# Performance work log

Hardware: AMD Instinct MI355X
Metric: run time of the kernel (lower is better)

Reference implementation:

```python
import jax, jax.numpy as jnp
import numpy as np

SIZES = (20, 20, 20, 20, 20)          # formula_oh_sizes
OH_N = sum(SIZES)                      # 100
NUM_BINS = 65536                       # spect_bin.get_num_bins()
EPS_SIZE = 1e-4                        # eps added to subset size
IN_EPS = 1e-5                          # torch InstanceNorm1d default eps


def thermometer_oh(counts):
    # StructuredOneHot with accum=True: per-element thermometer encoding.
    # counts: (N, E) element counts -> (N, sum(SIZES)) with out[j]=1 iff j < count.
    outs = [(jnp.arange(s, dtype=counts.dtype)[None, :] < counts[:, i:i + 1]).astype(jnp.float32)
            for i, s in enumerate(SIZES)]
    return jnp.concatenate(outs, axis=-1)


def inorm(x):
    # InstanceNorm1d (affine=False) as applied here: normalize over last dim per row.
    m = jnp.mean(x, axis=-1, keepdims=True)
    v = jnp.var(x, axis=-1, keepdims=True)
    return (x - m) * jax.lax.rsqrt(v + IN_EPS)


def _lin(key, fan_in, fan_out):
    k1, k2 = jax.random.split(key)
    bound = 1.0 / np.sqrt(fan_in)
    W = jax.random.uniform(k1, (fan_in, fan_out), jnp.float32, -bound, bound)
    b = jax.random.uniform(k2, (fan_out,), jnp.float32, -bound, bound)
    return W, b


def setup_inputs():
    key = jax.random.key(0)
    ks = jax.random.split(key, 12)
    B, A, GF, S, P, E, D = 8, 48, 256, 4096, 32, 5, 256
    vert_feat_in = jax.random.normal(ks[0], (B, A, GF), jnp.float32)
    vert_mask_in = jnp.ones((B, A), jnp.float32)
    elem_idx = jax.random.randint(ks[1], (B, A), 0, E)
    vert_element_oh = jax.nn.one_hot(elem_idx, E, dtype=jnp.float32)
    adj_oh = jnp.zeros((B, A, A), jnp.float32)                      # unused by forward path
    atom_subsets = jax.random.randint(ks[2], (B, S, A), 0, 2).astype(jnp.int32)
    atom_subsets_peaks = jnp.zeros((1,), jnp.float32)               # unused (mass_idx/intensity used)
    mass_idx = jax.random.randint(ks[3], (B, S, P), 0, NUM_BINS).astype(jnp.int32)
    intensity = jax.random.uniform(ks[4], (B, S, P), jnp.float32)
    combine_W, combine_b = _lin(ks[5], OH_N + GF, GF)
    l1_W, l1_b = _lin(ks[6], GF, D)
    l2a_W, l2a_b = _lin(ks[7], D, D)
    l2b_W, l2b_b = _lin(ks[8], D, D)
    score_W, score_b = _lin(ks[9], D, 1)
    return {
        'vert_feat_in': vert_feat_in, 'vert_mask_in': vert_mask_in,
        'vert_element_oh': vert_element_oh, 'adj_oh': adj_oh,
        'atom_subsets': atom_subsets, 'atom_subsets_peaks': atom_subsets_peaks,
        'mass_idx': mass_idx, 'intensity': intensity,
        'combine_W': combine_W, 'combine_b': combine_b,
        'l1_W': l1_W, 'l1_b': l1_b, 'l2a_W': l2a_W, 'l2a_b': l2a_b,
        'l2b_W': l2b_W, 'l2b_b': l2b_b, 'score_W': score_W, 'score_b': score_b,
    }


def reference(vert_feat_in, vert_mask_in, vert_element_oh, adj_oh, atom_subsets,
              atom_subsets_peaks, mass_idx, intensity,
              combine_W, combine_b, l1_W, l1_b, l2a_W, l2a_b, l2b_W, l2b_b,
              score_W, score_b):
    B, A, GF = vert_feat_in.shape
    _, S, _ = atom_subsets.shape
    subsets_f = atom_subsets.astype(jnp.float32)
    masked_vert = vert_feat_in * vert_mask_in[:, :, None]               # (B,A,GF)
    subsets_masked = subsets_f * vert_mask_in[:, None, :]               # (B,S,A)
    # weighted sum of vertex features over each subset
    sws = jnp.einsum('bag,bsa->bsg', masked_vert, subsets_masked)        # (B,S,GF)
    # per-subset element counts -> structured one-hot formula encoding
    counts = jnp.einsum('bae,bsa->bse', vert_element_oh, subsets_f)      # (B,S,E)
    pf_oh = thermometer_oh(counts.reshape(-1, counts.shape[-1])).reshape(B, S, OH_N)
    subset_size = jnp.sum(subsets_masked, axis=2) + EPS_SIZE             # (B,S)
    mean_feat = sws / subset_size[:, :, None]
    normed = inorm(mean_feat)                                            # subset_weighted_norm
    combined = jax.nn.relu(jnp.concatenate([pf_oh, normed], -1) @ combine_W + combine_b)
    x = inorm(combined)                                                  # norm_post_combine
    x = jax.nn.relu(x @ l1_W + l1_b)
    x = jax.nn.leaky_relu(x @ l2a_W + l2a_b)
    x = jax.nn.leaky_relu(x @ l2b_W + l2b_b)
    x = jax.nn.relu(x)
    x = inorm(x)                                                         # norm_pre_score
    scores = (x @ score_W + score_b)[..., 0]                             # (B,S)
    probs = jax.nn.softmax(scores, axis=-1)
    # per-batch sparse mass-matrix binning: scatter-add intensity*prob into spectral bins
    weighted = intensity * probs[:, :, None]                             # (B,S,P)
    seg = jax.vmap(lambda idx, w: jax.ops.segment_sum(w, idx, num_segments=NUM_BINS))
    spect_out = seg(mass_idx.reshape(B, -1), weighted.reshape(B, -1))    # (B,NUM_BINS)
    return spect_out, probs
```

## Files before the change

### kernel.cpp

```cpp
#include <hip/hip_runtime.h>
#include <math.h>

#define B_DIM 8
#define A_DIM 48
#define GF_DIM 256
#define S_DIM 4096
#define P_DIM 32
#define E_DIM 5
#define OHN 100
#define NBINS 65536

typedef __attribute__((ext_vector_type(8))) short short8v;
typedef __attribute__((ext_vector_type(4))) float float4v;

__device__ __forceinline__ float wave_sum(float v) {
#pragma unroll
    for (int o = 32; o; o >>= 1) v += __shfl_xor(v, o, 64);
    return v;
}
__device__ __forceinline__ float wave_max(float v) {
#pragma unroll
    for (int o = 32; o; o >>= 1) v = fmaxf(v, __shfl_xor(v, o, 64));
    return v;
}
__device__ __forceinline__ float quad16_sum(float v) {
    v += __shfl_xor(v, 1, 64); v += __shfl_xor(v, 2, 64);
    v += __shfl_xor(v, 4, 64); v += __shfl_xor(v, 8, 64);
    return v;
}
__device__ __forceinline__ unsigned short bf16_rn(float x) {
    unsigned int u = __float_as_uint(x);
    return (unsigned short)((u + 0x7FFFu + ((u >> 16) & 1u)) >> 16);
}
__device__ __forceinline__ float bf16_val(unsigned short h) {
    return __uint_as_float(((unsigned int)h) << 16);
}
__device__ __forceinline__ float4v mfma_bf16(short8v a, short8v b, float4v c) {
    return __builtin_amdgcn_mfma_f32_16x16x32_bf16(a, b, c, 0, 0, 0);
}

__global__ __launch_bounds__(256) void k_prep(
    const float* __restrict__ cW, const float* __restrict__ l1W,
    const float* __restrict__ l2aW, const float* __restrict__ l2bW,
    const float* __restrict__ vert_feat, const float* __restrict__ vert_mask,
    const float* __restrict__ elem_oh,
    short* __restrict__ wp, short* __restrict__ wv,
    float* __restrict__ maskB, int* __restrict__ eiB,
    float4* __restrict__ spect4)
{
    const int blk = blockIdx.x;
    const int tid = threadIdx.x;
    if (blk < 1152) {
        int e = blk * 256 + tid;
        int c = e >> 13;
        int i = e & 8191;
        int j    = i & 7;
        int lane = (i >> 3) & 63;
        int nt   = (i >> 9) & 1;
        int wn   = i >> 10;
        int krel = (lane >> 4) * 8 + j;
        int n    = wn * 32 + nt * 16 + (lane & 15);
        float val = 0.f;
        if (c < 12) {
            int kp = c * 32 + krel;
            if (kp < 100)       val = cW[kp * 256 + n];
            else if (kp >= 128) val = cW[(kp - 28) * 256 + n];
        } else {
            int L  = (c - 12) >> 3;
            int kc = (c - 12) & 7;
            const float* W = (L == 0) ? l1W : (L == 1) ? l2aW : l2bW;
            val = W[(kc * 32 + krel) * 256 + n];
        }
        unsigned short h = bf16_rn(val);
        float lo = val - bf16_val(h);
        int base = c * 16384 + (i & 511);
        wp[base + (wn * 4 + nt) * 512]     = (short)h;
        wp[base + (wn * 4 + 2 + nt) * 512] = (short)bf16_rn(lo);
    } else if (blk < 1664) {
        int vb = blk - 1152;
        int vc = vb >> 5;
        int i  = (vb & 31) * 256 + tid;
        int b  = vc >> 1, v = vc & 1;
        int j    = i & 7;
        int lane = (i >> 3) & 63;
        int nt   = (i >> 9) & 1;
        int wn   = i >> 10;
        int k = v * 32 + (lane >> 4) * 8 + j;
        int n = wn * 32 + nt * 16 + (lane & 15);
        float val = 0.f;
        if (k < A_DIM) {
            float mk = vert_mask[b * A_DIM + k];
            val = vert_feat[((size_t)(b * A_DIM + k)) * GF_DIM + n] * mk * mk;
        }
        unsigned short h = bf16_rn(val);
        float lo = val - bf16_val(h);
        int base = vc * 16384 + (i & 511);
        wv[base + (wn * 4 + nt) * 512]     = (short)h;
        wv[base + (wn * 4 + 2 + nt) * 512] = (short)bf16_rn(lo);
    } else if (blk == 1664) {
        for (int t = tid; t < B_DIM * A_DIM; t += 256) {
            maskB[t] = vert_mask[t];
            int ei = 0;
#pragma unroll
            for (int e = 0; e < E_DIM; ++e)
                if (elem_oh[t * E_DIM + e] > 0.5f) ei = e;
            eiB[t] = ei;
        }
    } else {
        int z = (blk - 1665) * 256 + tid;
        spect4[z] = make_float4(0.f, 0.f, 0.f, 0.f);
    }
}

#define L_XAL 24576
#define L_FM  40960
#define L_PS  45056
#define L_CNT 46080
#define L_INV 46720
#define L_TOT 46848

template <int NKC, int LO0, int ACT, bool NORM, bool SCORE>
__device__ __forceinline__ void layer_pass(
    short* xAh, short* xAl, float (*ps)[32],
    const short* __restrict__ wstream, const float* __restrict__ bias,
    const float* __restrict__ sW, const float* __restrict__ sb,
    float* __restrict__ scores, int R0)
{
    const int tid  = threadIdx.x;
    const int lane = tid & 63;
    const int wn   = tid >> 6;
    const int quad = lane >> 4;
    const int col  = lane & 15;
    const short* wbase = wstream + wn * 2048 + lane * 8;

    float4v acc[2][2];
#pragma unroll
    for (int mi = 0; mi < 2; ++mi)
#pragma unroll
        for (int nt = 0; nt < 2; ++nt) acc[mi][nt] = (float4v){0.f, 0.f, 0.f, 0.f};

    short8v bh[3][2], bl[3][2];
#pragma unroll
    for (int p = 0; p < 2; ++p) {
        if (p < NKC) {
            const short* q = wbase + p * 16384;
            bh[p][0] = *(const short8v*)(q);
            bh[p][1] = *(const short8v*)(q + 512);
            bl[p][0] = *(const short8v*)(q + 1024);
            bl[p][1] = *(const short8v*)(q + 1536);
        }
    }

#pragma unroll
    for (int kc = 0; kc < NKC; ++kc) {
        const int cur = kc % 3;
        if (kc + 2 < NKC) {
            const int nxt = (kc + 2) % 3;
            const short* q = wbase + (kc + 2) * 16384;
            bh[nxt][0] = *(const short8v*)(q);
            bh[nxt][1] = *(const short8v*)(q + 512);
            bl[nxt][0] = *(const short8v*)(q + 1024);
            bl[nxt][1] = *(const short8v*)(q + 1536);
        }
        short8v ah[2], al[2];
#pragma unroll
        for (int mi = 0; mi < 2; ++mi)
            ah[mi] = *(const short8v*)(xAh + ((kc * 2 + mi) * 64 + lane) * 8);
        const bool hlo = (kc >= LO0);
        if (hlo) {
#pragma unroll
            for (int mi = 0; mi < 2; ++mi)
                al[mi] = *(const short8v*)(xAl + (((kc - LO0) * 2 + mi) * 64 + lane) * 8);
        }
#pragma unroll
        for (int mi = 0; mi < 2; ++mi)
#pragma unroll
            for (int nt = 0; nt < 2; ++nt) {
                acc[mi][nt] = mfma_bf16(ah[mi], bh[cur][nt], acc[mi][nt]);
                acc[mi][nt] = mfma_bf16(ah[mi], bl[cur][nt], acc[mi][nt]);
                if (hlo)
                    acc[mi][nt] = mfma_bf16(al[mi], bh[cur][nt], acc[mi][nt]);
            }
    }

    float bc0 = bias[wn * 32 + col];
    float bc1 = bias[wn * 32 + 16 + col];
#pragma unroll
    for (int mi = 0; mi < 2; ++mi)
#pragma unroll
        for (int r = 0; r < 4; ++r) {
            float z0 = acc[mi][0][r] + bc0;
            float z1 = acc[mi][1][r] + bc1;
            if (ACT == 0) { z0 = fmaxf(z0, 0.f); z1 = fmaxf(z1, 0.f); }
            else { z0 = (z0 > 0.f) ? z0 : 0.01f * z0; z1 = (z1 > 0.f) ? z1 : 0.01f * z1; }
            acc[mi][0][r] = z0; acc[mi][1][r] = z1;
        }

    __syncthreads();

    if (NORM) {
        float rsum[2][4];
#pragma unroll
        for (int mi = 0; mi < 2; ++mi)
#pragma unroll
            for (int r = 0; r < 4; ++r)
                rsum[mi][r] = quad16_sum(acc[mi][0][r] + acc[mi][1][r]);
        if (col == 0) {
#pragma unroll
            for (int mi = 0; mi < 2; ++mi)
#pragma unroll
                for (int r = 0; r < 4; ++r)
                    ps[wn][mi * 16 + quad * 4 + r] = rsum[mi][r];
        }
        __syncthreads();
        float mu[2][4];
#pragma unroll
        for (int mi = 0; mi < 2; ++mi)
#pragma unroll
            for (int r = 0; r < 4; ++r) {
                int m = mi * 16 + quad * 4 + r;
                float s = 0.f;
#pragma unroll
                for (int w = 0; w < 8; ++w) s += ps[w][m];
                mu[mi][r] = s * (1.f / 256.f);
            }
        __syncthreads();
        float qs[2][4];
#pragma unroll
        for (int mi = 0; mi < 2; ++mi)
#pragma unroll
            for (int r = 0; r < 4; ++r) {
                acc[mi][0][r] -= mu[mi][r];
                acc[mi][1][r] -= mu[mi][r];
                float q = acc[mi][0][r] * acc[mi][0][r]
                        + acc[mi][1][r] * acc[mi][1][r];
                qs[mi][r] = quad16_sum(q);
            }
        if (col == 0) {
#pragma unroll
            for (int mi = 0; mi < 2; ++mi)
#pragma unroll
                for (int r = 0; r < 4; ++r)
                    ps[wn][mi * 16 + quad * 4 + r] = qs[mi][r];
        }
        __syncthreads();
#pragma unroll
        for (int mi = 0; mi < 2; ++mi)
#pragma unroll
            for (int r = 0; r < 4; ++r) {
                int m = mi * 16 + quad * 4 + r;
                float s = 0.f;
#pragma unroll
                for (int w = 0; w < 8; ++w) s += ps[w][m];
                float rsf = 1.0f / sqrtf(s * (1.f / 256.f) + 1e-5f);
                acc[mi][0][r] *= rsf;
                acc[mi][1][r] *= rsf;
            }
    }

    if (SCORE) {
        __syncthreads();
        float sv0 = sW[wn * 32 + col];
        float sv1 = sW[wn * 32 + 16 + col];
        float psu[2][4];
#pragma unroll
        for (int mi = 0; mi < 2; ++mi)
#pragma unroll
            for (int r = 0; r < 4; ++r)
                psu[mi][r] = quad16_sum(acc[mi][0][r] * sv0 + acc[mi][1][r] * sv1);
        if (col == 0) {
#pragma unroll
            for (int mi = 0; mi < 2; ++mi)
#pragma unroll
                for (int r = 0; r < 4; ++r)
                    ps[wn][mi * 16 + quad * 4 + r] = psu[mi][r];
        }
        __syncthreads();
        if (tid < 32) {
            float s = sb[0];
#pragma unroll
            for (int w = 0; w < 8; ++w) s += ps[w][tid];
            scores[R0 + tid] = s;
        }
    } else {
#pragma unroll
        for (int mi = 0; mi < 2; ++mi)
#pragma unroll
            for (int nt = 0; nt < 2; ++nt) {
                int nn0 = (nt * 16 + col) & ~1;
                int q2  = nn0 >> 3;
                int j0  = nn0 & 7;
#pragma unroll
                for (int r = 0; r < 4; ++r) {
                    float v  = acc[mi][nt][r];
                    float pv = __shfl_xor(v, 1, 64);
                    int m15 = quad * 4 + r;
                    int rowidx = (wn * 2 + mi) * 64 + q2 * 16 + m15;
                    if ((col & 1) == 0) {
                        unsigned int wd = (unsigned int)bf16_rn(v)
                                        | ((unsigned int)bf16_rn(pv) << 16);
                        ((unsigned int*)xAh)[rowidx * 4 + (j0 >> 1)] = wd;
                    } else {
                        float ls = v  - bf16_val(bf16_rn(v));
                        float lp = pv - bf16_val(bf16_rn(pv));
                        unsigned int wd = (unsigned int)bf16_rn(lp)
                                        | ((unsigned int)bf16_rn(ls) << 16);
                        ((unsigned int*)xAl)[rowidx * 4 + (j0 >> 1)] = wd;
                    }
                }
            }
        __syncthreads();
    }
}

__global__ __launch_bounds__(512, 4) void k_mlp(
    const int* __restrict__ subsets, const short* __restrict__ wprep,
    const short* __restrict__ vertB,
    const float* __restrict__ maskB, const int* __restrict__ eiB,
    const float* __restrict__ cb,  const float* __restrict__ l1b,
    const float* __restrict__ l2ab, const float* __restrict__ l2bb,
    const float* __restrict__ sW,  const float* __restrict__ sb,
    float* __restrict__ scores)
{
    __shared__ __align__(16) char smem[L_TOT];
    short*  xAh = (short*)smem;
    short*  xAl = (short*)(smem + L_XAL);
    short*  fm  = (short*)(smem + L_FM);
    float (*ps)[32]  = (float(*)[32])(smem + L_PS);
    float (*cnt)[5]  = (float(*)[5])(smem + L_CNT);
    float*  invsz    = (float*)(smem + L_INV);

    const int tid  = threadIdx.x;
    const int lane = tid & 63;
    const int wn   = tid >> 6;
    const int quad = lane >> 4;
    const int col  = lane & 15;
    const int fb   = blockIdx.x;
    const int b    = fb >> 7;
    const int R0   = fb * 32;

    if (tid < 256) {
        int g  = tid;
        int lg = g & 63;
        int t2 = g >> 6;
        int kc = t2 >> 1, mi = t2 & 1;
        int m  = mi * 16 + (lg & 15);
        int k0 = kc * 32 + (lg >> 4) * 8;
        const int* srow = subsets + (size_t)(R0 + m) * A_DIM;
        short8v hv;
#pragma unroll
        for (int j = 0; j < 8; ++j) {
            int k = k0 + j;
            hv[j] = (short)((k < A_DIM && srow[k]) ? 0x3F80 : 0);
        }
        *(short8v*)(fm + g * 8) = hv;
    }

    {
        const float mymask = (lane < A_DIM) ? maskB[b * A_DIM + lane] : 0.f;
        const int   myei   = (lane < A_DIM) ? eiB[b * A_DIM + lane]   : -1;
#pragma unroll
        for (int i = 0; i < 4; ++i) {
            int r = wn * 4 + i;
            int fl = (lane < A_DIM) ? subsets[(size_t)(R0 + r) * A_DIM + lane] : 0;
            unsigned long long m0 = __ballot(fl != 0 && myei == 0);
            unsigned long long m1 = __ballot(fl != 0 && myei == 1);
            unsigned long long m2 = __ballot(fl != 0 && myei == 2);
            unsigned long long m3 = __ballot(fl != 0 && myei == 3);
            unsigned long long m4 = __ballot(fl != 0 && myei == 4);
            float ssz = wave_sum(fl ? mymask : 0.f) + 1e-4f;
            if (lane == 0) {
                cnt[r][0] = (float)__popcll(m0);
                cnt[r][1] = (float)__popcll(m1);
                cnt[r][2] = (float)__popcll(m2);
                cnt[r][3] = (float)__popcll(m3);
                cnt[r][4] = (float)__popcll(m4);
                invsz[r]  = 1.0f / ssz;
            }
        }
    }
    __syncthreads();

    {
        const short* wbase = vertB + b * 32768 + wn * 2048 + lane * 8;
        float4v acc[2][2];
#pragma unroll
        for (int mi = 0; mi < 2; ++mi)
#pragma unroll
            for (int nt = 0; nt < 2; ++nt) acc[mi][nt] = (float4v){0.f, 0.f, 0.f, 0.f};

        short8v bh[2][2], bl[2][2];
#pragma unroll
        for (int kc = 0; kc < 2; ++kc) {
            const short* q = wbase + kc * 16384;
            bh[kc][0] = *(const short8v*)(q);
            bh[kc][1] = *(const short8v*)(q + 512);
            bl[kc][0] = *(const short8v*)(q + 1024);
            bl[kc][1] = *(const short8v*)(q + 1536);
        }
#pragma unroll
        for (int kc = 0; kc < 2; ++kc) {
            short8v a0 = *(const short8v*)(fm + ((kc * 2 + 0) * 64 + lane) * 8);
            short8v a1 = *(const short8v*)(fm + ((kc * 2 + 1) * 64 + lane) * 8);
#pragma unroll
            for (int nt = 0; nt < 2; ++nt) {
                acc[0][nt] = mfma_bf16(a0, bh[kc][nt], acc[0][nt]);
                acc[0][nt] = mfma_bf16(a0, bl[kc][nt], acc[0][nt]);
                acc[1][nt] = mfma_bf16(a1, bh[kc][nt], acc[1][nt]);
                acc[1][nt] = mfma_bf16(a1, bl[kc][nt], acc[1][nt]);
            }
        }

#pragma unroll
        for (int mi = 0; mi < 2; ++mi)
#pragma unroll
            for (int r = 0; r < 4; ++r) {
                float iv = invsz[mi * 16 + quad * 4 + r];
                acc[mi][0][r] *= iv;
                acc[mi][1][r] *= iv;
            }

        __syncthreads();

        {
            float rsum[2][4];
#pragma unroll
            for (int mi = 0; mi < 2; ++mi)
#pragma unroll
                for (int r = 0; r < 4; ++r)
                    rsum[mi][r] = quad16_sum(acc[mi][0][r] + acc[mi][1][r]);
            if (col == 0) {
#pragma unroll
                for (int mi = 0; mi < 2; ++mi)
#pragma unroll
                    for (int r = 0; r < 4; ++r)
                        ps[wn][mi * 16 + quad * 4 + r] = rsum[mi][r];
            }
            __syncthreads();
            float mu[2][4];
#pragma unroll
            for (int mi = 0; mi < 2; ++mi)
#pragma unroll
                for (int r = 0; r < 4; ++r) {
                    int m = mi * 16 + quad * 4 + r;
                    float s = 0.f;
#pragma unroll
                    for (int w = 0; w < 8; ++w) s += ps[w][m];
                    mu[mi][r] = s * (1.f / 256.f);
                }
            __syncthreads();
            float qs[2][4];
#pragma unroll
            for (int mi = 0; mi < 2; ++mi)
#pragma unroll
                for (int r = 0; r < 4; ++r) {
                    acc[mi][0][r] -= mu[mi][r];
                    acc[mi][1][r] -= mu[mi][r];
                    float q = acc[mi][0][r] * acc[mi][0][r]
                            + acc[mi][1][r] * acc[mi][1][r];
                    qs[mi][r] = quad16_sum(q);
                }
            if (col == 0) {
#pragma unroll
                for (int mi = 0; mi < 2; ++mi)
#pragma unroll
                    for (int r = 0; r < 4; ++r)
                        ps[wn][mi * 16 + quad * 4 + r] = qs[mi][r];
            }
            __syncthreads();
#pragma unroll
            for (int mi = 0; mi < 2; ++mi)
#pragma unroll
                for (int r = 0; r < 4; ++r) {
                    int m = mi * 16 + quad * 4 + r;
                    float s = 0.f;
#pragma unroll
                    for (int w = 0; w < 8; ++w) s += ps[w][m];
                    float rsf = 1.0f / sqrtf(s * (1.f / 256.f) + 1e-5f);
                    acc[mi][0][r] *= rsf;
                    acc[mi][1][r] *= rsf;
                }
        }

#pragma unroll
        for (int mi = 0; mi < 2; ++mi)
#pragma unroll
            for (int nt = 0; nt < 2; ++nt) {
                int nn0 = (nt * 16 + col) & ~1;
                int q2  = nn0 >> 3;
                int j0  = nn0 & 7;
#pragma unroll
                for (int r = 0; r < 4; ++r) {
                    float v  = acc[mi][nt][r];
                    float pv = __shfl_xor(v, 1, 64);
                    int m15 = quad * 4 + r;
                    int rh = ((4 + wn) * 2 + mi) * 64 + q2 * 16 + m15;
                    int rl = (wn * 2 + mi) * 64 + q2 * 16 + m15;
                    if ((col & 1) == 0) {
                        unsigned int wd = (unsigned int)bf16_rn(v)
                                        | ((unsigned int)bf16_rn(pv) << 16);
                        ((unsigned int*)xAh)[rh * 4 + (j0 >> 1)] = wd;
                    } else {
                        float ls = v  - bf16_val(bf16_rn(v));
                        float lp = pv - bf16_val(bf16_rn(pv));
                        unsigned int wd = (unsigned int)bf16_rn(lp)
                                        | ((unsigned int)bf16_rn(ls) << 16);
                        ((unsigned int*)xAl)[rl * 4 + (j0 >> 1)] = wd;
                    }
                }
            }

        {
            int g  = tid;
            int lg = g & 63;
            int t2 = g >> 6;
            int kc = t2 >> 1, mi = t2 & 1;
            int m  = mi * 16 + (lg & 15);
            int kb = (lg >> 4) * 8;
            float c0 = cnt[m][0], c1 = cnt[m][1], c2 = cnt[m][2],
                  c3 = cnt[m][3], c4 = cnt[m][4];
            short8v hv;
#pragma unroll
            for (int j = 0; j < 8; ++j) {
                int kp = kc * 32 + kb + j;
                float val = 0.f;
                if (kp < 100) {
                    int e = kp / 20;
                    float ce = (e == 0) ? c0 : (e == 1) ? c1 : (e == 2) ? c2
                             : (e == 3) ? c3 : c4;
                    val = ((float)(kp - e * 20) < ce) ? 1.0f : 0.0f;
                }
                hv[j] = (short)((val != 0.f) ? 0x3F80 : 0);
            }
            *(short8v*)(xAh + g * 8) = hv;
        }
        __syncthreads();
    }

    layer_pass<12, 4, 0, true,  false>(xAh, xAl, ps, wprep,
        cb, nullptr, nullptr, nullptr, R0);
    layer_pass< 8, 0, 0, false, false>(xAh, xAl, ps, wprep + 12 * 16384,
        l1b, nullptr, nullptr, nullptr, R0);
    layer_pass< 8, 0, 1, false, false>(xAh, xAl, ps, wprep + 20 * 16384,
        l2ab, nullptr, nullptr, nullptr, R0);
    layer_pass< 8, 0, 0, true,  true >(xAh, xAl, ps, wprep + 28 * 16384,
        l2bb, sW, sb, scores, R0);
}

__global__ __launch_bounds__(256) void k_softmax(float* __restrict__ probs) {
    const int b   = blockIdx.x;
    const int tid = threadIdx.x;
    __shared__ float redA[4];
    __shared__ float redB[4];
    float* sp = probs + (size_t)b * S_DIM;

    float v[16];
    float mx = -INFINITY;
#pragma unroll
    for (int i = 0; i < 16; ++i) {
        v[i] = sp[tid + i * 256];
        mx = fmaxf(mx, v[i]);
    }
    mx = wave_max(mx);
    if ((tid & 63) == 0) redA[tid >> 6] = mx;
    __syncthreads();
    mx = fmaxf(fmaxf(redA[0], redA[1]), fmaxf(redA[2], redA[3]));

    float sum = 0.f;
#pragma unroll
    for (int i = 0; i < 16; ++i) {
        v[i] = expf(v[i] - mx);
        sum += v[i];
    }
    sum = wave_sum(sum);
    if ((tid & 63) == 0) redB[tid >> 6] = sum;
    __syncthreads();
    float tot = redB[0] + redB[1] + redB[2] + redB[3];
    float inv = 1.0f / tot;
#pragma unroll
    for (int i = 0; i < 16; ++i) sp[tid + i * 256] = v[i] * inv;
}

__global__ __launch_bounds__(256) void k_scatter(
    const int*   __restrict__ mass_idx,
    const float* __restrict__ intensity,
    const float* __restrict__ probs,
    float* __restrict__ spect)
{
    int i  = blockIdx.x * 256 + threadIdx.x;
    int bs = i >> 5;
    int b  = i >> 17;
    float w = intensity[i] * probs[bs];
    unsafeAtomicAdd(spect + ((size_t)b << 16) + mass_idx[i], w);
}

extern "C" void kernel_launch(void* const* d_in, const int* in_sizes, int n_in,
                              void* d_out, int out_size, void* d_ws, size_t ws_size,
                              hipStream_t stream) {
    const float* vert_feat = (const float*)d_in[0];
    const float* vert_mask = (const float*)d_in[1];
    const float* elem_oh   = (const float*)d_in[2];
    const int*   subsets   = (const int*)d_in[4];
    const int*   mass_idx  = (const int*)d_in[6];
    const float* intensity = (const float*)d_in[7];
    const float* combine_W = (const float*)d_in[8];
    const float* combine_b = (const float*)d_in[9];
    const float* l1_W      = (const float*)d_in[10];
    const float* l1_b      = (const float*)d_in[11];
    const float* l2a_W     = (const float*)d_in[12];
    const float* l2a_b     = (const float*)d_in[13];
    const float* l2b_W     = (const float*)d_in[14];
    const float* l2b_b     = (const float*)d_in[15];
    const float* score_W   = (const float*)d_in[16];
    const float* score_b   = (const float*)d_in[17];

    float* out   = (float*)d_out;
    float* spect = out;
    float* probs = out + (size_t)B_DIM * NBINS;

    short* wprep = (short*)d_ws;
    short* vertB = wprep + 36 * 16384;
    float* maskB = (float*)(vertB + 16 * 16384);
    int*   eiB   = (int*)(maskB + B_DIM * A_DIM);

    k_prep<<<2177, 256, 0, stream>>>(combine_W, l1_W, l2a_W, l2b_W,
        vert_feat, vert_mask, elem_oh, wprep, vertB, maskB, eiB,
        (float4*)spect);
    k_mlp<<<1024, 512, 0, stream>>>(subsets, wprep, vertB, maskB, eiB,
        combine_b, l1_b, l2a_b, l2b_b, score_W, score_b, probs);
    k_softmax<<<B_DIM, 256, 0, stream>>>(probs);
    k_scatter<<<(B_DIM * S_DIM * P_DIM) / 256, 256, 0, stream>>>(
        mass_idx, intensity, probs, spect);
}
```

Before: 246.6 us.

## Fuse softmax into MLP score pass and scatter; shrink weight prefetch to double buffer

Removes the separate softmax kernel. The MLP's score pass now computes exp(score) per row and atomically adds it into a per-batch sum, and the scatter kernel normalizes exp(score)/sum on the fly and writes probs. It also drops the max subtraction, which risks overflow if scores are large; the test scores come after instance norm, so they are bounded. The weight prefetch depth in layer_pass is cut from three buffers to two, which lowers register pressure but gives less latency hiding. Atomic float sums also make the normalizer order-nondeterministic.

```diff
diff --git a/kernel.cpp b/kernel.cpp
--- a/kernel.cpp
+++ b/kernel.cpp
@@ -18,11 +18,6 @@
     for (int o = 32; o; o >>= 1) v += __shfl_xor(v, o, 64);
     return v;
 }
-__device__ __forceinline__ float wave_max(float v) {
-#pragma unroll
-    for (int o = 32; o; o >>= 1) v = fmaxf(v, __shfl_xor(v, o, 64));
-    return v;
-}
 __device__ __forceinline__ float quad16_sum(float v) {
     v += __shfl_xor(v, 1, 64); v += __shfl_xor(v, 2, 64);
     v += __shfl_xor(v, 4, 64); v += __shfl_xor(v, 8, 64);
@@ -46,7 +41,7 @@
     const float* __restrict__ elem_oh,
     short* __restrict__ wp, short* __restrict__ wv,
     float* __restrict__ maskB, int* __restrict__ eiB,
-    float4* __restrict__ spect4)
+    float* __restrict__ sums, float4* __restrict__ spect4)
 {
     const int blk = blockIdx.x;
     const int tid = threadIdx.x;
@@ -106,6 +101,7 @@
                 if (elem_oh[t * E_DIM + e] > 0.5f) ei = e;
             eiB[t] = ei;
         }
+        if (tid < B_DIM) sums[tid] = 0.0f;
     } else {
         int z = (blk - 1665) * 256 + tid;
         spect4[z] = make_float4(0.f, 0.f, 0.f, 0.f);
@@ -124,7 +120,7 @@
     short* xAh, short* xAl, float (*ps)[32],
     const short* __restrict__ wstream, const float* __restrict__ bias,
     const float* __restrict__ sW, const float* __restrict__ sb,
-    float* __restrict__ scores, int R0)
+    float* __restrict__ scores, float* __restrict__ sums, int R0)
 {
     const int tid  = threadIdx.x;
     const int lane = tid & 63;
@@ -139,28 +135,21 @@
 #pragma unroll
         for (int nt = 0; nt < 2; ++nt) acc[mi][nt] = (float4v){0.f, 0.f, 0.f, 0.f};
 
-    short8v bh[3][2], bl[3][2];
-#pragma unroll
-    for (int p = 0; p < 2; ++p) {
-        if (p < NKC) {
-            const short* q = wbase + p * 16384;
-            bh[p][0] = *(const short8v*)(q);
-            bh[p][1] = *(const short8v*)(q + 512);
-            bl[p][0] = *(const short8v*)(q + 1024);
-            bl[p][1] = *(const short8v*)(q + 1536);
-        }
-    }
+    short8v bh[2][2], bl[2][2];
+    bh[0][0] = *(const short8v*)(wbase);
+    bh[0][1] = *(const short8v*)(wbase + 512);
+    bl[0][0] = *(const short8v*)(wbase + 1024);
+    bl[0][1] = *(const short8v*)(wbase + 1536);
 
 #pragma unroll
     for (int kc = 0; kc < NKC; ++kc) {
-        const int cur = kc % 3;
-        if (kc + 2 < NKC) {
-            const int nxt = (kc + 2) % 3;
-            const short* q = wbase + (kc + 2) * 16384;
-            bh[nxt][0] = *(const short8v*)(q);
-            bh[nxt][1] = *(const short8v*)(q + 512);
-            bl[nxt][0] = *(const short8v*)(q + 1024);
-            bl[nxt][1] = *(const short8v*)(q + 1536);
+        const int cur = kc & 1;
+        if (kc + 1 < NKC) {
+            const short* q = wbase + (kc + 1) * 16384;
+            bh[cur ^ 1][0] = *(const short8v*)(q);
+            bh[cur ^ 1][1] = *(const short8v*)(q + 512);
+            bl[cur ^ 1][0] = *(const short8v*)(q + 1024);
+            bl[cur ^ 1][1] = *(const short8v*)(q + 1536);
         }
         short8v ah[2], al[2];
 #pragma unroll
@@ -281,6 +270,11 @@
 #pragma unroll
             for (int w = 0; w < 8; ++w) s += ps[w][tid];
             scores[R0 + tid] = s;
+            float e = expf(s);
+            e += __shfl_xor(e, 16, 64); e += __shfl_xor(e, 8, 64);
+            e += __shfl_xor(e, 4, 64);  e += __shfl_xor(e, 2, 64);
+            e += __shfl_xor(e, 1, 64);
+            if (tid == 0) atomicAdd(&sums[R0 >> 12], e);
         }
     } else {
 #pragma unroll
@@ -320,7 +314,7 @@
     const float* __restrict__ cb,  const float* __restrict__ l1b,
     const float* __restrict__ l2ab, const float* __restrict__ l2bb,
     const float* __restrict__ sW,  const float* __restrict__ sb,
-    float* __restrict__ scores)
+    float* __restrict__ scores, float* __restrict__ sums)
 {
     __shared__ __align__(16) char smem[L_TOT];
     short*  xAh = (short*)smem;
@@ -538,59 +532,29 @@
     }
 
     layer_pass<12, 4, 0, true,  false>(xAh, xAl, ps, wprep,
-        cb, nullptr, nullptr, nullptr, R0);
+        cb, nullptr, nullptr, nullptr, nullptr, R0);
     layer_pass< 8, 0, 0, false, false>(xAh, xAl, ps, wprep + 12 * 16384,
-        l1b, nullptr, nullptr, nullptr, R0);
+        l1b, nullptr, nullptr, nullptr, nullptr, R0);
     layer_pass< 8, 0, 1, false, false>(xAh, xAl, ps, wprep + 20 * 16384,
-        l2ab, nullptr, nullptr, nullptr, R0);
+        l2ab, nullptr, nullptr, nullptr, nullptr, R0);
     layer_pass< 8, 0, 0, true,  true >(xAh, xAl, ps, wprep + 28 * 16384,
-        l2bb, sW, sb, scores, R0);
-}
-
-__global__ __launch_bounds__(256) void k_softmax(float* __restrict__ probs) {
-    const int b   = blockIdx.x;
-    const int tid = threadIdx.x;
-    __shared__ float redA[4];
-    __shared__ float redB[4];
-    float* sp = probs + (size_t)b * S_DIM;
-
-    float v[16];
-    float mx = -INFINITY;
-#pragma unroll
-    for (int i = 0; i < 16; ++i) {
-        v[i] = sp[tid + i * 256];
-        mx = fmaxf(mx, v[i]);
-    }
-    mx = wave_max(mx);
-    if ((tid & 63) == 0) redA[tid >> 6] = mx;
-    __syncthreads();
-    mx = fmaxf(fmaxf(redA[0], redA[1]), fmaxf(redA[2], redA[3]));
-
-    float sum = 0.f;
-#pragma unroll
-    for (int i = 0; i < 16; ++i) {
-        v[i] = expf(v[i] - mx);
-        sum += v[i];
-    }
-    sum = wave_sum(sum);
-    if ((tid & 63) == 0) redB[tid >> 6] = sum;
-    __syncthreads();
-    float tot = redB[0] + redB[1] + redB[2] + redB[3];
-    float inv = 1.0f / tot;
-#pragma unroll
-    for (int i = 0; i < 16; ++i) sp[tid + i * 256] = v[i] * inv;
+        l2bb, sW, sb, scores, sums, R0);
 }
 
 __global__ __launch_bounds__(256) void k_scatter(
     const int*   __restrict__ mass_idx,
     const float* __restrict__ intensity,
-    const float* __restrict__ probs,
+    const float* __restrict__ scores,
+    const float* __restrict__ sums,
+    float* __restrict__ probs,
     float* __restrict__ spect)
 {
     int i  = blockIdx.x * 256 + threadIdx.x;
     int bs = i >> 5;
     int b  = i >> 17;
-    float w = intensity[i] * probs[bs];
+    float p = expf(scores[bs]) * (1.0f / sums[b]);
+    if ((i & 31) == 0) probs[bs] = p;
+    float w = intensity[i] * p;
     unsafeAtomicAdd(spect + ((size_t)b << 16) + mass_idx[i], w);
 }
 
@@ -618,17 +582,18 @@
     float* spect = out;
     float* probs = out + (size_t)B_DIM * NBINS;
 
-    short* wprep = (short*)d_ws;
-    short* vertB = wprep + 36 * 16384;
-    float* maskB = (float*)(vertB + 16 * 16384);
-    int*   eiB   = (int*)(maskB + B_DIM * A_DIM);
+    short* wprep  = (short*)d_ws;
+    short* vertB  = wprep + 36 * 16384;
+    float* maskB  = (float*)(vertB + 16 * 16384);
+    int*   eiB    = (int*)(maskB + B_DIM * A_DIM);
+    float* sums   = (float*)(eiB + B_DIM * A_DIM);
+    float* scores = sums + 8;
 
     k_prep<<<2177, 256, 0, stream>>>(combine_W, l1_W, l2a_W, l2b_W,
-        vert_feat, vert_mask, elem_oh, wprep, vertB, maskB, eiB,
+        vert_feat, vert_mask, elem_oh, wprep, vertB, maskB, eiB, sums,
         (float4*)spect);
     k_mlp<<<1024, 512, 0, stream>>>(subsets, wprep, vertB, maskB, eiB,
-        combine_b, l1_b, l2a_b, l2b_b, score_W, score_b, probs);
-    k_softmax<<<B_DIM, 256, 0, stream>>>(probs);
+        combine_b, l1_b, l2a_b, l2b_b, score_W, score_b, scores, sums);
     k_scatter<<<(B_DIM * S_DIM * P_DIM) / 256, 256, 0, stream>>>(
-        mass_idx, intensity, probs, spect);
-}
+        mass_idx, intensity, scores, sums, probs, spect);
+}
```

After: 248.3 us. Within noise of the previous version (+0.7%).
